# Kernel tuning notes

Hardware: AMD Instinct MI355X
Metric: run time of the kernel (lower is better)

The kernel has to match this reference:

```python
import jax, jax.numpy as jnp
import numpy as np

IN_FEATURES = 256
OUT_FEATURES = 512
NUM_SEGMENTS = 8
GRID_MIN, GRID_MAX = -1.0, 1.0
STEP = (GRID_MAX - GRID_MIN) / NUM_SEGMENTS
LN_EPS = 1e-5


def setup_inputs() -> dict:
    key = jax.random.key(0)
    k1, k2 = jax.random.split(key)
    B = 2048
    x = jax.random.normal(k1, (B, IN_FEATURES), dtype=jnp.float32)
    # Xavier-uniform a_embed, zeros b_embed, as in reset_parameters
    vocab = IN_FEATURES * NUM_SEGMENTS
    limit = float(np.sqrt(6.0 / (vocab + OUT_FEATURES)))
    a_weight = jax.random.uniform(k2, (vocab, OUT_FEATURES), minval=-limit, maxval=limit, dtype=jnp.float32)
    b_weight = jnp.zeros((vocab, OUT_FEATURES), dtype=jnp.float32)
    gamma = jnp.ones((IN_FEATURES,), dtype=jnp.float32)
    beta = jnp.zeros((IN_FEATURES,), dtype=jnp.float32)
    return {"x": x, "a_weight": a_weight, "b_weight": b_weight, "gamma": gamma, "beta": beta}


def reference(x, a_weight, b_weight, gamma, beta):
    # LayerNorm over in_features
    mu = jnp.mean(x, axis=-1, keepdims=True)
    var = jnp.mean(jnp.square(x - mu), axis=-1, keepdims=True)
    xn = (x - mu) * jax.lax.rsqrt(var + LN_EPS) * gamma + beta  # [B, I]

    # data-dependent segment index (torch .long() truncates; clamp makes trunc==floor here)
    float_idx = (xn - GRID_MIN) / STEP
    seg = jnp.clip(float_idx.astype(jnp.int32), 0, NUM_SEGMENTS - 1)  # [B, I]
    global_idx = seg + jnp.arange(IN_FEATURES, dtype=jnp.int32)[None, :] * NUM_SEGMENTS

    a_vals = a_weight[global_idx]  # [B, I, O]
    b_vals = b_weight[global_idx]  # [B, I, O]
    # sum over in_features of a*x + b
    y = jnp.einsum('bi,bio->bo', xn, a_vals) + jnp.sum(b_vals, axis=1)
    return y
```

## Files before the change

### kernel.cpp

```cpp
#include <hip/hip_runtime.h>

#define I_FEAT 256
#define O_FEAT 512
#define NSEG   8
#define KDIM   (I_FEAT * NSEG)
#define KTOT   (2 * KDIM)
#define KC_N   (KTOT / 32)

typedef _Float16 half8   __attribute__((ext_vector_type(8)));
typedef float    floatx4 __attribute__((ext_vector_type(4)));
typedef uint32_t uintx4  __attribute__((ext_vector_type(4)));

__global__ __launch_bounds__(256) void prep(
    const float* __restrict__ x,
    const float* __restrict__ Aw,
    const float* __restrict__ Bw,
    const float* __restrict__ gamma,
    const float* __restrict__ beta,
    uint4* __restrict__ Bf,
    uint2* __restrict__ Am,
    int Bn, int pbTot)
{
    __shared__ uint32_t smem[16 * 260];
    const int t   = threadIdx.x;
    const int bid = blockIdx.x;

    if (bid < pbTot) {
        unsigned short (*T)[72] = (unsigned short(*)[72])smem;
        const int n0 = (bid & 7) * 64;
        const int k0 = (bid >> 3) * 64;
        const float* src = (k0 < KDIM) ? (Aw + (size_t)k0 * O_FEAT)
                                       : (Bw + (size_t)(k0 - KDIM) * O_FEAT);
        #pragma unroll
        for (int s = 0; s < 4; ++s) {
            int e  = s * 1024 + t * 4;
            int kl = e >> 6, nl = e & 63;
            const float4 v = *(const float4*)(src + (size_t)kl * O_FEAT + n0 + nl);
            T[nl + 0][kl] = __builtin_bit_cast(unsigned short, (_Float16)v.x);
            T[nl + 1][kl] = __builtin_bit_cast(unsigned short, (_Float16)v.y);
            T[nl + 2][kl] = __builtin_bit_cast(unsigned short, (_Float16)v.z);
            T[nl + 3][kl] = __builtin_bit_cast(unsigned short, (_Float16)v.w);
        }
        __syncthreads();

        const int lane = t & 63, lane16 = lane & 15, quad = lane >> 4;
        const int sub  = t >> 6;
        #pragma unroll
        for (int f = 0; f < 2; ++f) {
            const int combo = sub * 2 + f;
            const int n16g  = combo & 3;
            const int kch   = combo >> 2;
            const int nl = n16g * 16 + lane16;
            const int kl = kch * 32 + quad * 8;
            const uint4 val = *(const uint4*)&T[nl][kl];
            const int n16t = (n0 >> 4) + n16g;
            const int kc   = (k0 >> 5) + kch;
            Bf[((size_t)n16t * KC_N + kc) * 64 + lane] = val;
        }
    } else {
        uint32_t (*M)[260] = (uint32_t(*)[260])smem;
        const int mt16 = bid - pbTot;
        const int rr   = t >> 4;
        const int c16  = t & 15;
        const int row  = mt16 * 16 + rr;
        const bool ok  = (row < Bn);

        float4 v[4];
        const float* xr = x + (size_t)row * I_FEAT + c16 * 16;
        #pragma unroll
        for (int j = 0; j < 4; ++j)
            v[j] = ok ? *(const float4*)(xr + j * 4) : make_float4(0.f, 0.f, 0.f, 0.f);

        float sum = 0.f, sq = 0.f;
        #pragma unroll
        for (int j = 0; j < 4; ++j) {
            sum += v[j].x + v[j].y + v[j].z + v[j].w;
            sq  += v[j].x * v[j].x + v[j].y * v[j].y
                 + v[j].z * v[j].z + v[j].w * v[j].w;
        }
        #pragma unroll
        for (int mask = 1; mask < 16; mask <<= 1) {
            sum += __shfl_xor(sum, mask);
            sq  += __shfl_xor(sq,  mask);
        }
        const float mu  = sum * (1.0f / I_FEAT);
        const float var = sq * (1.0f / I_FEAT) - mu * mu;
        const float rs  = rsqrtf(var + 1e-5f);

        #pragma unroll
        for (int j = 0; j < 4; ++j) {
            const float4 g4 = *(const float4*)(gamma + c16 * 16 + j * 4);
            const float4 b4 = *(const float4*)(beta  + c16 * 16 + j * 4);
            const float vv[4] = { v[j].x, v[j].y, v[j].z, v[j].w };
            const float gg[4] = { g4.x, g4.y, g4.z, g4.w };
            const float bb[4] = { b4.x, b4.y, b4.z, b4.w };
            #pragma unroll
            for (int e = 0; e < 4; ++e) {
                const int c = c16 * 16 + j * 4 + e;
                float xn = (vv[e] - mu) * rs * gg[e] + bb[e];
                float fi = (xn + 1.0f) * 4.0f;
                int seg = (int)fi;
                seg = seg < 0 ? 0 : (seg > NSEG - 1 ? NSEG - 1 : seg);
                _Float16 hx = (_Float16)xn;
                M[rr][c] = ((uint32_t)seg << 16)
                         | (uint32_t)__builtin_bit_cast(unsigned short, hx);
            }
        }
        __syncthreads();

        const int lane = t & 63, g = t >> 6;
        const int m_local = lane & 15, quad = lane >> 4;
        uint2* dst = Am + (size_t)mt16 * 64 * 64 + lane;
        #pragma unroll
        for (int kk = 0; kk < 16; ++kk) {
            const int kcp = g * 16 + kk;
            const int w0  = kcp * 8 + quad;
            const int w1  = w0 + 4;
            const uint32_t u0 = M[m_local][w0 & 255];
            const uint32_t u1 = M[m_local][w1 & 255];
            const uint32_t a  = (w0 >> 8) ? ((u0 & 0xFFFF0000u) | 0x3C00u) : u0;
            const uint32_t b  = (w1 >> 8) ? ((u1 & 0xFFFF0000u) | 0x3C00u) : u1;
            dst[(size_t)kcp * 64] = make_uint2(a, b);
        }
    }
}

static __device__ __forceinline__ half8 build_onehot(uint32_t u) {
    const uint32_t xb  = u & 0xFFFFu;
    const uint32_t seg = u >> 16;
    const uint64_t oh  = (uint64_t)xb << ((seg & 3u) << 4);
    const uint64_t lo  = (seg < 4u) ? oh : 0ull;
    const uint64_t hi  = (seg < 4u) ? 0ull : oh;
    uintx4 w;
    w[0] = (uint32_t)lo; w[1] = (uint32_t)(lo >> 32);
    w[2] = (uint32_t)hi; w[3] = (uint32_t)(hi >> 32);
    return __builtin_bit_cast(half8, w);
}

__global__ __launch_bounds__(512, 2) void kan_gemm(
    const uint2* __restrict__ Am,
    const uint4* __restrict__ Bf,
    float* __restrict__ out,
    int Bn)
{
    __shared__ uint4 bbuf[2][32][64];

    const int t      = threadIdx.x;
    const int wave   = t >> 6, lane = t & 63;
    const int wm     = wave >> 1;
    const int wn     = wave & 1;
    const int lane16 = lane & 15, quad = lane >> 4;

    const int nb = blockIdx.x;
    const int mb = blockIdx.y;

    const uint2* pa = Am + ((size_t)(mb * 4 + wm) * 64) * 64 + lane;

    floatx4 acc0 = {}, acc1 = {};

    auto stage = [&](int s, int b) {
        const int kc0 = s * 8;
        #pragma unroll
        for (int j = 0; j < 4; ++j) {
            const int idx  = j * 8 + wave;
            const int n16l = idx >> 3, kcl = idx & 7;
            const uint4* g = Bf
                + ((size_t)((nb * 4 + n16l) * KC_N + kc0 + kcl)) * 64 + lane;
            __builtin_amdgcn_global_load_lds(
                (const __attribute__((address_space(1))) uint32_t*)g,
                (__attribute__((address_space(3))) uint32_t*)&bbuf[b][idx][lane],
                16, 0, 0);
        }
    };

    uint2 cur[4], nxt[4];
    stage(0, 0);
    #pragma unroll
    for (int c = 0; c < 4; ++c) cur[c] = pa[(size_t)c * 64];
    __syncthreads();

    for (int s = 0; s < 16; ++s) {
        const int b = s & 1;
        if (s < 15) {
            stage(s + 1, b ^ 1);
            #pragma unroll
            for (int c = 0; c < 4; ++c) nxt[c] = pa[(size_t)((s + 1) * 4 + c) * 64];
        }
        #pragma unroll
        for (int c = 0; c < 4; ++c) {
            const int kcl0 = c * 2;
            const half8 b00 = __builtin_bit_cast(half8, bbuf[b][(wn * 2 + 0) * 8 + kcl0][lane]);
            const half8 b10 = __builtin_bit_cast(half8, bbuf[b][(wn * 2 + 1) * 8 + kcl0][lane]);
            const half8 b01 = __builtin_bit_cast(half8, bbuf[b][(wn * 2 + 0) * 8 + kcl0 + 1][lane]);
            const half8 b11 = __builtin_bit_cast(half8, bbuf[b][(wn * 2 + 1) * 8 + kcl0 + 1][lane]);
            half8 a = build_onehot(cur[c].x);
            acc0 = __builtin_amdgcn_mfma_f32_16x16x32_f16(a, b00, acc0, 0, 0, 0);
            acc1 = __builtin_amdgcn_mfma_f32_16x16x32_f16(a, b10, acc1, 0, 0, 0);
            a = build_onehot(cur[c].y);
            acc0 = __builtin_amdgcn_mfma_f32_16x16x32_f16(a, b01, acc0, 0, 0, 0);
            acc1 = __builtin_amdgcn_mfma_f32_16x16x32_f16(a, b11, acc1, 0, 0, 0);
        }
        __syncthreads();
        #pragma unroll
        for (int c = 0; c < 4; ++c) cur[c] = nxt[c];
    }

    const int grow0 = mb * 64 + wm * 16 + quad * 4;
    const int gcol  = nb * 64 + wn * 32 + lane16;
    #pragma unroll
    for (int r = 0; r < 4; ++r) {
        const int grow = grow0 + r;
        if (grow < Bn) {
            out[(size_t)grow * O_FEAT + gcol]      = acc0[r];
            out[(size_t)grow * O_FEAT + gcol + 16] = acc1[r];
        }
    }
}

extern "C" void kernel_launch(void* const* d_in, const int* in_sizes, int n_in,
                              void* d_out, int out_size, void* d_ws, size_t ws_size,
                              hipStream_t stream) {
    const float* x   = (const float*)d_in[0];
    const float* Aw  = (const float*)d_in[1];
    const float* Bw  = (const float*)d_in[2];
    const float* gam = (const float*)d_in[3];
    const float* bet = (const float*)d_in[4];
    float* out       = (float*)d_out;

    const int Bn      = in_sizes[0] / I_FEAT;
    const int mt16Tot = (Bn + 15) / 16;
    const int mb64Tot = (Bn + 63) / 64;
    const int pbTot   = (O_FEAT / 64) * (KTOT / 64);

    uint4* Bf = (uint4*)d_ws;
    uint2* Am = (uint2*)(Bf + (size_t)(O_FEAT / 16) * KC_N * 64);

    hipLaunchKernelGGL(prep, dim3(pbTot + mt16Tot), dim3(256), 0, stream,
                       x, Aw, Bw, gam, bet, Bf, Am, Bn, pbTot);
    hipLaunchKernelGGL(kan_gemm, dim3(O_FEAT / 64, mb64Tot), dim3(512), 0, stream,
                       Am, Bf, out, Bn);
}
```

Before: 89.00 us.

## Fuse LayerNorm/segment encoding into GEMM and split K across wave groups

Moves the LayerNorm and segment-index packing out of the prep kernel and into the GEMM kernel, where each block normalizes its 64 rows into shared memory, so the packed A operand is no longer written to or read from global memory. The GEMM now has two wave groups splitting the K chunks of each stage, with each wave computing a 32x32 tile, and a shared-memory reduction at the end. The price is about 66KB of extra LDS per block, with launch bounds lowered to one block per SM. The LayerNorm is also recomputed by each of the 8 N-blocks.

```diff
diff --git a/kernel.cpp b/kernel.cpp
--- a/kernel.cpp
+++ b/kernel.cpp
@@ -12,116 +12,42 @@
 typedef uint32_t uintx4  __attribute__((ext_vector_type(4)));
 
 __global__ __launch_bounds__(256) void prep(
-    const float* __restrict__ x,
     const float* __restrict__ Aw,
     const float* __restrict__ Bw,
-    const float* __restrict__ gamma,
-    const float* __restrict__ beta,
-    uint4* __restrict__ Bf,
-    uint2* __restrict__ Am,
-    int Bn, int pbTot)
+    uint4* __restrict__ Bf)
 {
-    __shared__ uint32_t smem[16 * 260];
+    __shared__ unsigned short T[64][72];
     const int t   = threadIdx.x;
     const int bid = blockIdx.x;
-
-    if (bid < pbTot) {
-        unsigned short (*T)[72] = (unsigned short(*)[72])smem;
-        const int n0 = (bid & 7) * 64;
-        const int k0 = (bid >> 3) * 64;
-        const float* src = (k0 < KDIM) ? (Aw + (size_t)k0 * O_FEAT)
-                                       : (Bw + (size_t)(k0 - KDIM) * O_FEAT);
-        #pragma unroll
-        for (int s = 0; s < 4; ++s) {
-            int e  = s * 1024 + t * 4;
-            int kl = e >> 6, nl = e & 63;
-            const float4 v = *(const float4*)(src + (size_t)kl * O_FEAT + n0 + nl);
-            T[nl + 0][kl] = __builtin_bit_cast(unsigned short, (_Float16)v.x);
-            T[nl + 1][kl] = __builtin_bit_cast(unsigned short, (_Float16)v.y);
-            T[nl + 2][kl] = __builtin_bit_cast(unsigned short, (_Float16)v.z);
-            T[nl + 3][kl] = __builtin_bit_cast(unsigned short, (_Float16)v.w);
-        }
-        __syncthreads();
-
-        const int lane = t & 63, lane16 = lane & 15, quad = lane >> 4;
-        const int sub  = t >> 6;
-        #pragma unroll
-        for (int f = 0; f < 2; ++f) {
-            const int combo = sub * 2 + f;
-            const int n16g  = combo & 3;
-            const int kch   = combo >> 2;
-            const int nl = n16g * 16 + lane16;
-            const int kl = kch * 32 + quad * 8;
-            const uint4 val = *(const uint4*)&T[nl][kl];
-            const int n16t = (n0 >> 4) + n16g;
-            const int kc   = (k0 >> 5) + kch;
-            Bf[((size_t)n16t * KC_N + kc) * 64 + lane] = val;
-        }
-    } else {
-        uint32_t (*M)[260] = (uint32_t(*)[260])smem;
-        const int mt16 = bid - pbTot;
-        const int rr   = t >> 4;
-        const int c16  = t & 15;
-        const int row  = mt16 * 16 + rr;
-        const bool ok  = (row < Bn);
-
-        float4 v[4];
-        const float* xr = x + (size_t)row * I_FEAT + c16 * 16;
-        #pragma unroll
-        for (int j = 0; j < 4; ++j)
-            v[j] = ok ? *(const float4*)(xr + j * 4) : make_float4(0.f, 0.f, 0.f, 0.f);
-
-        float sum = 0.f, sq = 0.f;
-        #pragma unroll
-        for (int j = 0; j < 4; ++j) {
-            sum += v[j].x + v[j].y + v[j].z + v[j].w;
-            sq  += v[j].x * v[j].x + v[j].y * v[j].y
-                 + v[j].z * v[j].z + v[j].w * v[j].w;
-        }
-        #pragma unroll
-        for (int mask = 1; mask < 16; mask <<= 1) {
-            sum += __shfl_xor(sum, mask);
-            sq  += __shfl_xor(sq,  mask);
-        }
-        const float mu  = sum * (1.0f / I_FEAT);
-        const float var = sq * (1.0f / I_FEAT) - mu * mu;
-        const float rs  = rsqrtf(var + 1e-5f);
-
-        #pragma unroll
-        for (int j = 0; j < 4; ++j) {
-            const float4 g4 = *(const float4*)(gamma + c16 * 16 + j * 4);
-            const float4 b4 = *(const float4*)(beta  + c16 * 16 + j * 4);
-            const float vv[4] = { v[j].x, v[j].y, v[j].z, v[j].w };
-            const float gg[4] = { g4.x, g4.y, g4.z, g4.w };
-            const float bb[4] = { b4.x, b4.y, b4.z, b4.w };
-            #pragma unroll
-            for (int e = 0; e < 4; ++e) {
-                const int c = c16 * 16 + j * 4 + e;
-                float xn = (vv[e] - mu) * rs * gg[e] + bb[e];
-                float fi = (xn + 1.0f) * 4.0f;
-                int seg = (int)fi;
-                seg = seg < 0 ? 0 : (seg > NSEG - 1 ? NSEG - 1 : seg);
-                _Float16 hx = (_Float16)xn;
-                M[rr][c] = ((uint32_t)seg << 16)
-                         | (uint32_t)__builtin_bit_cast(unsigned short, hx);
-            }
-        }
-        __syncthreads();
-
-        const int lane = t & 63, g = t >> 6;
-        const int m_local = lane & 15, quad = lane >> 4;
-        uint2* dst = Am + (size_t)mt16 * 64 * 64 + lane;
-        #pragma unroll
-        for (int kk = 0; kk < 16; ++kk) {
-            const int kcp = g * 16 + kk;
-            const int w0  = kcp * 8 + quad;
-            const int w1  = w0 + 4;
-            const uint32_t u0 = M[m_local][w0 & 255];
-            const uint32_t u1 = M[m_local][w1 & 255];
-            const uint32_t a  = (w0 >> 8) ? ((u0 & 0xFFFF0000u) | 0x3C00u) : u0;
-            const uint32_t b  = (w1 >> 8) ? ((u1 & 0xFFFF0000u) | 0x3C00u) : u1;
-            dst[(size_t)kcp * 64] = make_uint2(a, b);
-        }
+    const int n0 = (bid & 7) * 64;
+    const int k0 = (bid >> 3) * 64;
+    const float* src = (k0 < KDIM) ? (Aw + (size_t)k0 * O_FEAT)
+                                   : (Bw + (size_t)(k0 - KDIM) * O_FEAT);
+    #pragma unroll
+    for (int s = 0; s < 4; ++s) {
+        int e  = s * 1024 + t * 4;
+        int kl = e >> 6, nl = e & 63;
+        const float4 v = *(const float4*)(src + (size_t)kl * O_FEAT + n0 + nl);
+        T[nl + 0][kl] = __builtin_bit_cast(unsigned short, (_Float16)v.x);
+        T[nl + 1][kl] = __builtin_bit_cast(unsigned short, (_Float16)v.y);
+        T[nl + 2][kl] = __builtin_bit_cast(unsigned short, (_Float16)v.z);
+        T[nl + 3][kl] = __builtin_bit_cast(unsigned short, (_Float16)v.w);
+    }
+    __syncthreads();
+
+    const int lane = t & 63, lane16 = lane & 15, quad = lane >> 4;
+    const int sub  = t >> 6;
+    #pragma unroll
+    for (int f = 0; f < 2; ++f) {
+        const int combo = sub * 2 + f;
+        const int n16g  = combo & 3;
+        const int kch   = combo >> 2;
+        const int nl = n16g * 16 + lane16;
+        const int kl = kch * 32 + quad * 8;
+        const uint4 val = *(const uint4*)&T[nl][kl];
+        const int n16t = (n0 >> 4) + n16g;
+        const int kc   = (k0 >> 5) + kch;
+        Bf[((size_t)n16t * KC_N + kc) * 64 + lane] = val;
     }
 }
 
@@ -137,26 +63,26 @@
     return __builtin_bit_cast(half8, w);
 }
 
-__global__ __launch_bounds__(512, 2) void kan_gemm(
-    const uint2* __restrict__ Am,
+__global__ __launch_bounds__(512, 1) void kan_gemm(
+    const float* __restrict__ x,
+    const float* __restrict__ gamma,
+    const float* __restrict__ beta,
     const uint4* __restrict__ Bf,
     float* __restrict__ out,
     int Bn)
 {
-    __shared__ uint4 bbuf[2][32][64];
+    __shared__ uint4    bbuf[2][32][64];
+    __shared__ uint32_t M[64][258];
 
     const int t      = threadIdx.x;
     const int wave   = t >> 6, lane = t & 63;
-    const int wm     = wave >> 1;
+    const int ks     = wave >> 2;
+    const int wm     = (wave >> 1) & 1;
     const int wn     = wave & 1;
     const int lane16 = lane & 15, quad = lane >> 4;
 
     const int nb = blockIdx.x;
     const int mb = blockIdx.y;
-
-    const uint2* pa = Am + ((size_t)(mb * 4 + wm) * 64) * 64 + lane;
-
-    floatx4 acc0 = {}, acc1 = {};
 
     auto stage = [&](int s, int b) {
         const int kc0 = s * 8;
@@ -173,46 +99,120 @@
         }
     };
 
-    uint2 cur[4], nxt[4];
     stage(0, 0);
-    #pragma unroll
-    for (int c = 0; c < 4; ++c) cur[c] = pa[(size_t)c * 64];
+
+    {
+        const int rl = t >> 3;
+        const int c8 = t & 7;
+        const int row = mb * 64 + rl;
+        const bool ok = (row < Bn);
+        const float* xr = x + (size_t)row * I_FEAT + c8 * 32;
+
+        float4 v[8];
+        #pragma unroll
+        for (int j = 0; j < 8; ++j)
+            v[j] = ok ? *(const float4*)(xr + j * 4) : make_float4(0.f, 0.f, 0.f, 0.f);
+
+        float sum = 0.f, sq = 0.f;
+        #pragma unroll
+        for (int j = 0; j < 8; ++j) {
+            sum += v[j].x + v[j].y + v[j].z + v[j].w;
+            sq  += v[j].x * v[j].x + v[j].y * v[j].y
+                 + v[j].z * v[j].z + v[j].w * v[j].w;
+        }
+        #pragma unroll
+        for (int mask = 1; mask < 8; mask <<= 1) {
+            sum += __shfl_xor(sum, mask);
+            sq  += __shfl_xor(sq,  mask);
+        }
+        const float mu  = sum * (1.0f / I_FEAT);
+        const float var = sq * (1.0f / I_FEAT) - mu * mu;
+        const float rs  = rsqrtf(var + 1e-5f);
+
+        #pragma unroll
+        for (int j = 0; j < 8; ++j) {
+            const int cb = c8 * 32 + j * 4;
+            const float4 g4 = *(const float4*)(gamma + cb);
+            const float4 b4 = *(const float4*)(beta  + cb);
+            const float vv[4] = { v[j].x, v[j].y, v[j].z, v[j].w };
+            const float gg[4] = { g4.x, g4.y, g4.z, g4.w };
+            const float bb[4] = { b4.x, b4.y, b4.z, b4.w };
+            #pragma unroll
+            for (int e = 0; e < 4; ++e) {
+                float xn = (vv[e] - mu) * rs * gg[e] + bb[e];
+                float fi = (xn + 1.0f) * 4.0f;
+                int seg = (int)fi;
+                seg = seg < 0 ? 0 : (seg > NSEG - 1 ? NSEG - 1 : seg);
+                _Float16 hx = (_Float16)xn;
+                M[rl][cb + e] = ((uint32_t)seg << 16)
+                              | (uint32_t)__builtin_bit_cast(unsigned short, hx);
+            }
+        }
+    }
     __syncthreads();
+
+    floatx4 acc[2][2] = {};
+    const int ml0 = wm * 32 + lane16;
 
     for (int s = 0; s < 16; ++s) {
         const int b = s & 1;
-        if (s < 15) {
-            stage(s + 1, b ^ 1);
+        if (s < 15) stage(s + 1, b ^ 1);
+        const uint32_t isBias = (s >= 8);
+
+        #pragma unroll
+        for (int c = 0; c < 4; ++c) {
+            const int kcl = ks * 4 + c;
+            const int kc  = s * 8 + kcl;
+            const int i   = (kc * 4 + quad) & 255;
+
+            const half8 b0 = __builtin_bit_cast(half8, bbuf[b][(wn * 2 + 0) * 8 + kcl][lane]);
+            const half8 b1 = __builtin_bit_cast(half8, bbuf[b][(wn * 2 + 1) * 8 + kcl][lane]);
+
+            uint32_t u0 = M[ml0][i];
+            uint32_t u1 = M[ml0 + 16][i];
+            if (isBias) {
+                u0 = (u0 & 0xFFFF0000u) | 0x3C00u;
+                u1 = (u1 & 0xFFFF0000u) | 0x3C00u;
+            }
+            const half8 a0 = build_onehot(u0);
+            const half8 a1 = build_onehot(u1);
+            acc[0][0] = __builtin_amdgcn_mfma_f32_16x16x32_f16(a0, b0, acc[0][0], 0, 0, 0);
+            acc[0][1] = __builtin_amdgcn_mfma_f32_16x16x32_f16(a0, b1, acc[0][1], 0, 0, 0);
+            acc[1][0] = __builtin_amdgcn_mfma_f32_16x16x32_f16(a1, b0, acc[1][0], 0, 0, 0);
+            acc[1][1] = __builtin_amdgcn_mfma_f32_16x16x32_f16(a1, b1, acc[1][1], 0, 0, 0);
+        }
+        __syncthreads();
+    }
+
+    float* red = (float*)bbuf;
+    const int slot = wm * 2 + wn;
+    if (ks == 1) {
+        #pragma unroll
+        for (int sm = 0; sm < 2; ++sm)
             #pragma unroll
-            for (int c = 0; c < 4; ++c) nxt[c] = pa[(size_t)((s + 1) * 4 + c) * 64];
-        }
-        #pragma unroll
-        for (int c = 0; c < 4; ++c) {
-            const int kcl0 = c * 2;
-            const half8 b00 = __builtin_bit_cast(half8, bbuf[b][(wn * 2 + 0) * 8 + kcl0][lane]);
-            const half8 b10 = __builtin_bit_cast(half8, bbuf[b][(wn * 2 + 1) * 8 + kcl0][lane]);
-            const half8 b01 = __builtin_bit_cast(half8, bbuf[b][(wn * 2 + 0) * 8 + kcl0 + 1][lane]);
-            const half8 b11 = __builtin_bit_cast(half8, bbuf[b][(wn * 2 + 1) * 8 + kcl0 + 1][lane]);
-            half8 a = build_onehot(cur[c].x);
-            acc0 = __builtin_amdgcn_mfma_f32_16x16x32_f16(a, b00, acc0, 0, 0, 0);
-            acc1 = __builtin_amdgcn_mfma_f32_16x16x32_f16(a, b10, acc1, 0, 0, 0);
-            a = build_onehot(cur[c].y);
-            acc0 = __builtin_amdgcn_mfma_f32_16x16x32_f16(a, b01, acc0, 0, 0, 0);
-            acc1 = __builtin_amdgcn_mfma_f32_16x16x32_f16(a, b11, acc1, 0, 0, 0);
-        }
-        __syncthreads();
-        #pragma unroll
-        for (int c = 0; c < 4; ++c) cur[c] = nxt[c];
-    }
-
-    const int grow0 = mb * 64 + wm * 16 + quad * 4;
-    const int gcol  = nb * 64 + wn * 32 + lane16;
-    #pragma unroll
-    for (int r = 0; r < 4; ++r) {
-        const int grow = grow0 + r;
-        if (grow < Bn) {
-            out[(size_t)grow * O_FEAT + gcol]      = acc0[r];
-            out[(size_t)grow * O_FEAT + gcol + 16] = acc1[r];
+            for (int sn = 0; sn < 2; ++sn)
+                #pragma unroll
+                for (int r = 0; r < 4; ++r)
+                    red[(slot * 16 + (sm * 2 + sn) * 4 + r) * 64 + lane] = acc[sm][sn][r];
+    }
+    __syncthreads();
+    if (ks == 0) {
+        #pragma unroll
+        for (int sm = 0; sm < 2; ++sm) {
+            const int grow0 = mb * 64 + wm * 32 + sm * 16 + quad * 4;
+            #pragma unroll
+            for (int sn = 0; sn < 2; ++sn) {
+                const int gcol = nb * 64 + wn * 32 + sn * 16 + lane16;
+                #pragma unroll
+                for (int r = 0; r < 4; ++r) {
+                    const int grow = grow0 + r;
+                    if (grow < Bn) {
+                        const float v = acc[sm][sn][r]
+                            + red[(slot * 16 + (sm * 2 + sn) * 4 + r) * 64 + lane];
+                        out[(size_t)grow * O_FEAT + gcol] = v;
+                    }
+                }
+            }
         }
     }
 }
@@ -228,15 +228,12 @@
     float* out       = (float*)d_out;
 
     const int Bn      = in_sizes[0] / I_FEAT;
-    const int mt16Tot = (Bn + 15) / 16;
     const int mb64Tot = (Bn + 63) / 64;
     const int pbTot   = (O_FEAT / 64) * (KTOT / 64);
 
     uint4* Bf = (uint4*)d_ws;
-    uint2* Am = (uint2*)(Bf + (size_t)(O_FEAT / 16) * KC_N * 64);
-
-    hipLaunchKernelGGL(prep, dim3(pbTot + mt16Tot), dim3(256), 0, stream,
-                       x, Aw, Bw, gam, bet, Bf, Am, Bn, pbTot);
+
+    hipLaunchKernelGGL(prep, dim3(pbTot), dim3(256), 0, stream, Aw, Bw, Bf);
     hipLaunchKernelGGL(kan_gemm, dim3(O_FEAT / 64, mb64Tot), dim3(512), 0, stream,
-                       Am, Bf, out, Bn);
-}
+                       x, gam, bet, Bf, out, Bn);
+}
```

After: 96.39 us. 8.3% more time.

## Split-K GEMM with register-direct B loads and separate partial-sum reduction

Applied to the files above, without the earlier changes.

Replaces the LDS double-buffered GEMM with a split-K scheme. Each 256-thread block computes a 128x64 output tile over one quarter of K, loading A and B fragments straight from global memory into registers, and writes partial sums to workspace. A new reduce kernel then adds the four partials. The aim is more blocks and more MFMAs per fragment load (a 2x4 tile per wave) without LDS barriers. In exchange it adds partial-sum traffic and a third kernel launch, and B fragments are re-read from global memory by each wave.

```diff
diff --git a/kernel.cpp b/kernel.cpp
--- a/kernel.cpp
+++ b/kernel.cpp
@@ -137,84 +137,116 @@
     return __builtin_bit_cast(half8, w);
 }
 
-__global__ __launch_bounds__(512, 2) void kan_gemm(
+__global__ __launch_bounds__(256, 2) void kan_gemm(
     const uint2* __restrict__ Am,
     const uint4* __restrict__ Bf,
-    float* __restrict__ out,
-    int Bn)
+    float* __restrict__ P,
+    int rt128Tot)
 {
-    __shared__ uint4 bbuf[2][32][64];
-
     const int t      = threadIdx.x;
     const int wave   = t >> 6, lane = t & 63;
-    const int wm     = wave >> 1;
-    const int wn     = wave & 1;
     const int lane16 = lane & 15, quad = lane >> 4;
 
-    const int nb = blockIdx.x;
-    const int mb = blockIdx.y;
-
-    const uint2* pa = Am + ((size_t)(mb * 4 + wm) * 64) * 64 + lane;
-
-    floatx4 acc0 = {}, acc1 = {};
-
-    auto stage = [&](int s, int b) {
-        const int kc0 = s * 8;
+    const int bid = blockIdx.x;
+    const int ot  = bid & 7;
+    const int rem = bid >> 3;
+    const int rt  = rem % rt128Tot;
+    const int kh  = rem / rt128Tot;
+
+    const uint2* pa0 = Am + ((size_t)(rt * 8 + wave * 2 + 0) * 64) * 64 + lane;
+    const uint2* pa1 = Am + ((size_t)(rt * 8 + wave * 2 + 1) * 64) * 64 + lane;
+    const uint4* pb0 = Bf + ((size_t)(ot * 4 + 0) * KC_N) * 64 + lane;
+    const uint4* pb1 = Bf + ((size_t)(ot * 4 + 1) * KC_N) * 64 + lane;
+    const uint4* pb2 = Bf + ((size_t)(ot * 4 + 2) * KC_N) * 64 + lane;
+    const uint4* pb3 = Bf + ((size_t)(ot * 4 + 3) * KC_N) * 64 + lane;
+
+    floatx4 acc[2][4] = {};
+    const int kcp0 = kh * 16;
+
+    #pragma unroll 4
+    for (int p = 0; p < 16; ++p) {
+        const int kcp = kcp0 + p;
+        const uint2 u0 = pa0[(size_t)kcp * 64];
+        const uint2 u1 = pa1[(size_t)kcp * 64];
+        const size_t o0 = (size_t)(2 * kcp) * 64;
+        const size_t o1 = o0 + 64;
+        const uint4 bv00 = pb0[o0], bv01 = pb0[o1];
+        const uint4 bv10 = pb1[o0], bv11 = pb1[o1];
+        const uint4 bv20 = pb2[o0], bv21 = pb2[o1];
+        const uint4 bv30 = pb3[o0], bv31 = pb3[o1];
+        {
+            const half8 a0 = build_onehot(u0.x);
+            const half8 a1 = build_onehot(u1.x);
+            const half8 n0 = __builtin_bit_cast(half8, bv00);
+            const half8 n1 = __builtin_bit_cast(half8, bv10);
+            const half8 n2 = __builtin_bit_cast(half8, bv20);
+            const half8 n3 = __builtin_bit_cast(half8, bv30);
+            acc[0][0] = __builtin_amdgcn_mfma_f32_16x16x32_f16(a0, n0, acc[0][0], 0, 0, 0);
+            acc[0][1] = __builtin_amdgcn_mfma_f32_16x16x32_f16(a0, n1, acc[0][1], 0, 0, 0);
+            acc[0][2] = __builtin_amdgcn_mfma_f32_16x16x32_f16(a0, n2, acc[0][2], 0, 0, 0);
+            acc[0][3] = __builtin_amdgcn_mfma_f32_16x16x32_f16(a0, n3, acc[0][3], 0, 0, 0);
+            acc[1][0] = __builtin_amdgcn_mfma_f32_16x16x32_f16(a1, n0, acc[1][0], 0, 0, 0);
+            acc[1][1] = __builtin_amdgcn_mfma_f32_16x16x32_f16(a1, n1, acc[1][1], 0, 0, 0);
+            acc[1][2] = __builtin_amdgcn_mfma_f32_16x16x32_f16(a1, n2, acc[1][2], 0, 0, 0);
+            acc[1][3] = __builtin_amdgcn_mfma_f32_16x16x32_f16(a1, n3, acc[1][3], 0, 0, 0);
+        }
+        {
+            const half8 a0 = build_onehot(u0.y);
+            const half8 a1 = build_onehot(u1.y);
+            const half8 n0 = __builtin_bit_cast(half8, bv01);
+            const half8 n1 = __builtin_bit_cast(half8, bv11);
+            const half8 n2 = __builtin_bit_cast(half8, bv21);
+            const half8 n3 = __builtin_bit_cast(half8, bv31);
+            acc[0][0] = __builtin_amdgcn_mfma_f32_16x16x32_f16(a0, n0, acc[0][0], 0, 0, 0);
+            acc[0][1] = __builtin_amdgcn_mfma_f32_16x16x32_f16(a0, n1, acc[0][1], 0, 0, 0);
+            acc[0][2] = __builtin_amdgcn_mfma_f32_16x16x32_f16(a0, n2, acc[0][2], 0, 0, 0);
+            acc[0][3] = __builtin_amdgcn_mfma_f32_16x16x32_f16(a0, n3, acc[0][3], 0, 0, 0);
+            acc[1][0] = __builtin_amdgcn_mfma_f32_16x16x32_f16(a1, n0, acc[1][0], 0, 0, 0);
+            acc[1][1] = __builtin_amdgcn_mfma_f32_16x16x32_f16(a1, n1, acc[1][1], 0, 0, 0);
+            acc[1][2] = __builtin_amdgcn_mfma_f32_16x16x32_f16(a1, n2, acc[1][2], 0, 0, 0);
+            acc[1][3] = __builtin_amdgcn_mfma_f32_16x16x32_f16(a1, n3, acc[1][3], 0, 0, 0);
+        }
+    }
+
+    float* pblk = P + (size_t)bid * (128 * 64);
+    #pragma unroll
+    for (int sm = 0; sm < 2; ++sm) {
+        const int ml0 = wave * 32 + sm * 16 + quad * 4;
         #pragma unroll
         for (int j = 0; j < 4; ++j) {
-            const int idx  = j * 8 + wave;
-            const int n16l = idx >> 3, kcl = idx & 7;
-            const uint4* g = Bf
-                + ((size_t)((nb * 4 + n16l) * KC_N + kc0 + kcl)) * 64 + lane;
-            __builtin_amdgcn_global_load_lds(
-                (const __attribute__((address_space(1))) uint32_t*)g,
-                (__attribute__((address_space(3))) uint32_t*)&bbuf[b][idx][lane],
-                16, 0, 0);
-        }
-    };
-
-    uint2 cur[4], nxt[4];
-    stage(0, 0);
-    #pragma unroll
-    for (int c = 0; c < 4; ++c) cur[c] = pa[(size_t)c * 64];
-    __syncthreads();
-
-    for (int s = 0; s < 16; ++s) {
-        const int b = s & 1;
-        if (s < 15) {
-            stage(s + 1, b ^ 1);
+            const int nl = j * 16 + lane16;
             #pragma unroll
-            for (int c = 0; c < 4; ++c) nxt[c] = pa[(size_t)((s + 1) * 4 + c) * 64];
-        }
-        #pragma unroll
-        for (int c = 0; c < 4; ++c) {
-            const int kcl0 = c * 2;
-            const half8 b00 = __builtin_bit_cast(half8, bbuf[b][(wn * 2 + 0) * 8 + kcl0][lane]);
-            const half8 b10 = __builtin_bit_cast(half8, bbuf[b][(wn * 2 + 1) * 8 + kcl0][lane]);
-            const half8 b01 = __builtin_bit_cast(half8, bbuf[b][(wn * 2 + 0) * 8 + kcl0 + 1][lane]);
-            const half8 b11 = __builtin_bit_cast(half8, bbuf[b][(wn * 2 + 1) * 8 + kcl0 + 1][lane]);
-            half8 a = build_onehot(cur[c].x);
-            acc0 = __builtin_amdgcn_mfma_f32_16x16x32_f16(a, b00, acc0, 0, 0, 0);
-            acc1 = __builtin_amdgcn_mfma_f32_16x16x32_f16(a, b10, acc1, 0, 0, 0);
-            a = build_onehot(cur[c].y);
-            acc0 = __builtin_amdgcn_mfma_f32_16x16x32_f16(a, b01, acc0, 0, 0, 0);
-            acc1 = __builtin_amdgcn_mfma_f32_16x16x32_f16(a, b11, acc1, 0, 0, 0);
-        }
-        __syncthreads();
-        #pragma unroll
-        for (int c = 0; c < 4; ++c) cur[c] = nxt[c];
+            for (int r = 0; r < 4; ++r)
+                pblk[(ml0 + r) * 64 + nl] = acc[sm][j][r];
+        }
     }
-
-    const int grow0 = mb * 64 + wm * 16 + quad * 4;
-    const int gcol  = nb * 64 + wn * 32 + lane16;
-    #pragma unroll
-    for (int r = 0; r < 4; ++r) {
-        const int grow = grow0 + r;
-        if (grow < Bn) {
-            out[(size_t)grow * O_FEAT + gcol]      = acc0[r];
-            out[(size_t)grow * O_FEAT + gcol + 16] = acc1[r];
-        }
-    }
+}
+
+__global__ __launch_bounds__(256) void reduceP(
+    const float* __restrict__ P,
+    float* __restrict__ out,
+    int Bn, int rt128Tot)
+{
+    const int gid = blockIdx.x * 256 + threadIdx.x;
+    const int e0  = gid * 4;
+    const int m   = e0 >> 9;
+    const int n   = e0 & 511;
+    if (m >= Bn) return;
+    const int rt = m >> 7, ml = m & 127;
+    const int ot = n >> 6, nl = n & 63;
+    const size_t base     = ((size_t)(rt * 8 + ot)) * 8192 + ml * 64 + nl;
+    const size_t khStride = (size_t)rt128Tot * 8 * 8192;
+
+    const float4 p0 = *(const float4*)(P + base);
+    const float4 p1 = *(const float4*)(P + base + khStride);
+    const float4 p2 = *(const float4*)(P + base + 2 * khStride);
+    const float4 p3 = *(const float4*)(P + base + 3 * khStride);
+    float4 s;
+    s.x = (p0.x + p1.x) + (p2.x + p3.x);
+    s.y = (p0.y + p1.y) + (p2.y + p3.y);
+    s.z = (p0.z + p1.z) + (p2.z + p3.z);
+    s.w = (p0.w + p1.w) + (p2.w + p3.w);
+    *(float4*)(out + e0) = s;
 }
 
 extern "C" void kernel_launch(void* const* d_in, const int* in_sizes, int n_in,
@@ -227,16 +259,19 @@
     const float* bet = (const float*)d_in[4];
     float* out       = (float*)d_out;
 
-    const int Bn      = in_sizes[0] / I_FEAT;
-    const int mt16Tot = (Bn + 15) / 16;
-    const int mb64Tot = (Bn + 63) / 64;
-    const int pbTot   = (O_FEAT / 64) * (KTOT / 64);
+    const int Bn       = in_sizes[0] / I_FEAT;
+    const int mt16Tot  = (Bn + 15) / 16;
+    const int rt128Tot = (Bn + 127) / 128;
+    const int pbTot    = (O_FEAT / 64) * (KTOT / 64);
 
     uint4* Bf = (uint4*)d_ws;
     uint2* Am = (uint2*)(Bf + (size_t)(O_FEAT / 16) * KC_N * 64);
+    float* P  = (float*)(Am + (size_t)mt16Tot * 64 * 64);
 
     hipLaunchKernelGGL(prep, dim3(pbTot + mt16Tot), dim3(256), 0, stream,
                        x, Aw, Bw, gam, bet, Bf, Am, Bn, pbTot);
-    hipLaunchKernelGGL(kan_gemm, dim3(O_FEAT / 64, mb64Tot), dim3(512), 0, stream,
-                       Am, Bf, out, Bn);
-}
+    hipLaunchKernelGGL(kan_gemm, dim3(8 * rt128Tot * 4), dim3(256), 0, stream,
+                       Am, Bf, P, rt128Tot);
+    hipLaunchKernelGGL(reduceP, dim3((Bn * O_FEAT / 4 + 255) / 256), dim3(256), 0, stream,
+                       P, out, Bn, rt128Tot);
+}
```

Result: slower. 91.15 us (+2.4%).
